# Optimization experiments

Measured on AMD Instinct MI355X. Metric: run time of the kernel, lower is better.

Reference implementation:

```python
import jax, jax.numpy as jnp
import numpy as np
from jax import lax

EPS = 1e-5

def _conv(x, w, stride=1, pad=0, groups=1):
    return lax.conv_general_dilated(
        x, w, (stride, stride), ((pad, pad), (pad, pad)),
        dimension_numbers=('NCHW', 'OIHW', 'NCHW'),
        feature_group_count=groups)

def _bn(x, gamma, beta):
    # BatchNorm2d, training-mode batch statistics (biased variance)
    mean = jnp.mean(x, axis=(0, 2, 3), keepdims=True)
    var = jnp.var(x, axis=(0, 2, 3), keepdims=True)
    xn = (x - mean) * lax.rsqrt(var + EPS)
    return xn * gamma[None, :, None, None] + beta[None, :, None, None]

def _silu(x):
    return x * jax.nn.sigmoid(x)

def setup_inputs() -> dict:
    key = jax.random.key(0)
    ks = jax.random.split(key, 20)
    B, C, H, W = 16, 128, 128, 128
    L2 = 100
    s = 0.05
    d = {
        'x': jax.random.normal(ks[0], (B, C, H, W), jnp.float32),
        'dce_output': jax.random.normal(ks[1], (B, L2, C), jnp.float32),
        # per-channel 3x3 convs fused as one depthwise conv [C,1,3,3]
        'dw_conv': jax.random.normal(ks[2], (C, 1, 3, 3), jnp.float32) * s,
        'W_dce1': jax.random.normal(ks[3], (L2 * C, C), jnp.float32) * s,
        'b_dce1': jnp.zeros((C,), jnp.float32),
        'W_dce2': jax.random.normal(ks[4], (C, C), jnp.float32) * s,
        'b_dce2': jnp.zeros((C,), jnp.float32),
        'W_sh': jax.random.normal(ks[5], (C, C // 2), jnp.float32) * s,
        'b_sh': jnp.zeros((C // 2,), jnp.float32),
        'W_ex': jax.random.normal(ks[6], (C // 2, C), jnp.float32) * s,
        'b_ex': jnp.zeros((C,), jnp.float32),
        'conv1_w': jax.random.normal(ks[7], (C, C, 3, 3), jnp.float32) * s,
        'bn1_g': jnp.ones((C,), jnp.float32),
        'bn1_b': jnp.zeros((C,), jnp.float32),
        'conv2_w': jax.random.normal(ks[8], (C, C, 1, 1), jnp.float32) * s,
        'bn2_g': jnp.ones((C,), jnp.float32),
        'bn2_b': jnp.zeros((C,), jnp.float32),
        'sc_w': jax.random.normal(ks[9], (C, C, 1, 1), jnp.float32) * s,
        'bnsc_g': jnp.ones((C,), jnp.float32),
        'bnsc_b': jnp.zeros((C,), jnp.float32),
    }
    return d

def reference(x, dce_output, dw_conv, W_dce1, b_dce1, W_dce2, b_dce2,
              W_sh, b_sh, W_ex, b_ex, conv1_w, bn1_g, bn1_b,
              conv2_w, bn2_g, bn2_b, sc_w, bnsc_g, bnsc_b):
    B, C, H, W = x.shape
    stride = 1
    # DCE FFN: Linear -> GELU(exact) -> Linear
    dce_flat = dce_output.reshape(B, -1)
    h = jax.nn.gelu(dce_flat @ W_dce1 + b_dce1, approximate=False)
    dce_features = h @ W_dce2 + b_dce2  # [B, C]
    # per-channel 3x3 conv + global avg pool, fused as depthwise conv
    sp = _conv(x, dw_conv, stride=1, pad=1, groups=C)
    spatial_features = jnp.mean(sp, axis=(2, 3))  # [B, C]
    # SE-style modulation
    m = dce_features * spatial_features
    shrunk = jax.nn.gelu(m @ W_sh + b_sh, approximate=False)
    mod_w = jax.nn.sigmoid(shrunk @ W_ex + b_ex)  # [B, C]
    xm = x * mod_w[:, :, None, None]
    # ResBlock
    bb = _bn(_conv(xm, conv1_w, stride=stride, pad=1), bn1_g, bn1_b)
    bb = _silu(bb)
    bb = _bn(_conv(bb, conv2_w, stride=1, pad=0), bn2_g, bn2_b)
    sc = _bn(_conv(xm, sc_w, stride=stride, pad=0), bnsc_g, bnsc_b)
    return _silu(bb + sc)
```

## Files before the change

kernel.cpp:

```cpp
#include <hip/hip_runtime.h>
#include <hip/hip_bf16.h>

typedef _Float16 f16;
typedef __attribute__((ext_vector_type(8))) _Float16 f16x8;
typedef __attribute__((ext_vector_type(4))) _Float16 f16x4;
typedef __attribute__((ext_vector_type(4))) float f32x4;

__device__ __forceinline__ float geluf(float x) {
    return 0.5f * x * (1.0f + erff(x * 0.70710678118654752440f));
}
__device__ __forceinline__ float sigmf(float x) { return 1.0f / (1.0f + __expf(-x)); }

#define NB 16
#define NC 128
#define NH 128
#define NW 128
#define PLANE (NH * NW)
#define NSTAT 262144.0f

__device__ __align__(16) f16 g_Wc[9 * 4 * 128 * 32];
__device__ __align__(16) f16 g_Wsc[4 * 128 * 32];
__device__ __align__(16) f16 g_W2[4 * 128 * 32];
__device__ __align__(16) f16 g_xmT[(size_t)16 * 128 * 4 * 130 * 32];
__device__ __align__(16) f16 g_y1T[(size_t)16 * 128 * 4 * 128 * 32];
__device__ __align__(16) f16 g_bbT[(size_t)16 * 128 * 4 * 128 * 32];

__global__ __launch_bounds__(256) void k_wprep(const float* __restrict__ c1w,
                                               const float* __restrict__ scw,
                                               const float* __restrict__ c2w) {
    int i = blockIdx.x * 256 + threadIdx.x;
    if (i < 147456) {
        int tap = i / 16384;
        int rem = i - tap * 16384;
        int chunk = rem >> 12;
        int r2 = rem & 4095;
        int co = r2 >> 5;
        int cil = r2 & 31;
        int ci = chunk * 32 + cil;
        g_Wc[i] = (f16)c1w[((size_t)co * 128 + ci) * 9 + tap];
    } else if (i < 163840) {
        int j = i - 147456;
        int chunk = j >> 12;
        int r2 = j & 4095;
        int co = r2 >> 5;
        int cil = r2 & 31;
        g_Wsc[j] = (f16)scw[(size_t)co * 128 + chunk * 32 + cil];
    } else if (i < 180224) {
        int j = i - 163840;
        int chunk = j >> 12;
        int r2 = j & 4095;
        int co = r2 >> 5;
        int cil = j & 31;
        g_W2[j] = (f16)c2w[(size_t)co * 128 + chunk * 32 + cil];
    }
}

__global__ __launch_bounds__(256) void k_dce1(const float* __restrict__ dce,
                                              const float* __restrict__ W1,
                                              float* __restrict__ dh) {
    int ks = blockIdx.x;
    int kbase = ks * 200;
    int t = threadIdx.x;
    __shared__ float sdce[16][256];
    for (int e = t; e < 4096; e += 256) {
        int bb = e >> 8, k = e & 255;
        if (k < 200) sdce[bb][k] = dce[(size_t)bb * 12800 + kbase + k];
    }
    __syncthreads();
    int j = t & 127;
    int bg = t >> 7;
    float accs[8];
#pragma unroll
    for (int i = 0; i < 8; ++i) accs[i] = 0.0f;
    for (int k = 0; k < 200; ++k) {
        float wv = W1[((size_t)(kbase + k)) * 128 + j];
#pragma unroll
        for (int bb = 0; bb < 8; ++bb) accs[bb] += sdce[bg * 8 + bb][k] * wv;
    }
#pragma unroll
    for (int bb = 0; bb < 8; ++bb)
        atomicAdd(&dh[(bg * 8 + bb) * 128 + j], accs[bb]);
}

__global__ __launch_bounds__(128) void k_dce2(const float* __restrict__ dh,
                                              const float* __restrict__ b1,
                                              const float* __restrict__ W2,
                                              const float* __restrict__ b2,
                                              float* __restrict__ feat) {
    int b = blockIdx.x, j = threadIdx.x;
    __shared__ float sh[128];
    sh[j] = geluf(dh[b * 128 + j] + b1[j]);
    __syncthreads();
    float acc = b2[j];
    for (int k = 0; k < 128; ++k) acc += sh[k] * W2[k * 128 + j];
    feat[b * 128 + j] = acc;
}

__global__ __launch_bounds__(256) void k_spatial(const float* __restrict__ x,
                                                 const float* __restrict__ dw,
                                                 float* __restrict__ spat) {
    int bc = blockIdx.x;
    int t = threadIdx.x;
    const float* p = x + (size_t)bc * PLANE;
    float f = 0, r0 = 0, r1 = 0, c0 = 0, c1 = 0;
    for (int i = t; i < PLANE; i += 256) {
        float v = p[i];
        int row = i >> 7, col = i & 127;
        f += v;
        if (row == 0) r0 += v;
        if (row == 127) r1 += v;
        if (col == 0) c0 += v;
        if (col == 127) c1 += v;
    }
#pragma unroll
    for (int o = 1; o < 64; o <<= 1) {
        f  += __shfl_xor(f, o);
        r0 += __shfl_xor(r0, o);
        r1 += __shfl_xor(r1, o);
        c0 += __shfl_xor(c0, o);
        c1 += __shfl_xor(c1, o);
    }
    __shared__ float wr[4][5];
    int wid = t >> 6;
    if ((t & 63) == 0) {
        wr[wid][0] = f; wr[wid][1] = r0; wr[wid][2] = r1; wr[wid][3] = c0; wr[wid][4] = c1;
    }
    __syncthreads();
    if (t == 0) {
        float full = 0, row0 = 0, row127 = 0, col0 = 0, col127 = 0;
#pragma unroll
        for (int w = 0; w < 4; ++w) {
            full += wr[w][0]; row0 += wr[w][1]; row127 += wr[w][2];
            col0 += wr[w][3]; col127 += wr[w][4];
        }
        int c = bc & 127;
        float x00 = p[0];
        float x0e = p[127];
        float xe0 = p[127 * 128];
        float xee = p[127 * 128 + 127];
        float acc = 0.0f;
        for (int kh = 0; kh < 3; ++kh)
            for (int kw = 0; kw < 3; ++kw) {
                int dh_ = kh - 1, dwv = kw - 1;
                float T = full;
                if (dh_ == -1) T -= row127;
                else if (dh_ == 1) T -= row0;
                if (dwv == -1) T -= col127;
                else if (dwv == 1) T -= col0;
                if (dh_ == -1 && dwv == -1) T += xee;
                if (dh_ == -1 && dwv == 1) T += xe0;
                if (dh_ == 1 && dwv == -1) T += x0e;
                if (dh_ == 1 && dwv == 1) T += x00;
                acc += dw[c * 9 + kh * 3 + kw] * T;
            }
        spat[bc] = acc * (1.0f / 16384.0f);
    }
}

__global__ __launch_bounds__(128) void k_mod(const float* __restrict__ feat,
                                             const float* __restrict__ spat,
                                             const float* __restrict__ Wsh,
                                             const float* __restrict__ bsh,
                                             const float* __restrict__ Wex,
                                             const float* __restrict__ bex,
                                             float* __restrict__ mod) {
    int b = blockIdx.x, t = threadIdx.x;
    __shared__ float sm[128], ssh[64];
    sm[t] = feat[b * 128 + t] * spat[b * 128 + t];
    __syncthreads();
    if (t < 64) {
        float acc = bsh[t];
        for (int c = 0; c < 128; ++c) acc += sm[c] * Wsh[c * 64 + t];
        ssh[t] = geluf(acc);
    }
    __syncthreads();
    float acc = bex[t];
    for (int k = 0; k < 64; ++k) acc += ssh[k] * Wex[k * 128 + t];
    mod[b * 128 + t] = sigmf(acc);
}

__global__ __launch_bounds__(256) void k_xprep(const float* __restrict__ x,
                                               const float* __restrict__ mod) {
    int bid = blockIdx.x;
    int h = bid & 127;
    int b = bid >> 7;
    int t = threadIdx.x;
    __shared__ float sx[32][133];

    for (int chunk = 0; chunk < 4; ++chunk) {
        __syncthreads();
#pragma unroll
        for (int it = 0; it < 4; ++it) {
            int ci = it * 8 + (t >> 5);
            int w4 = t & 31;
            int cig = chunk * 32 + ci;
            float4 v = *(const float4*)&x[(((size_t)b * 128 + cig) * 128 + h) * 128 + w4 * 4];
            float m = mod[b * 128 + cig];
            sx[ci][w4 * 4 + 0] = v.x * m;
            sx[ci][w4 * 4 + 1] = v.y * m;
            sx[ci][w4 * 4 + 2] = v.z * m;
            sx[ci][w4 * 4 + 3] = v.w * m;
        }
        __syncthreads();
        f16* dstc = g_xmT + (((size_t)(b * 128 + h)) * 4 + chunk) * 4160;
        for (int g = t; g < 520; g += 256) {
            int s = g >> 2, c8 = g & 3;
            f16x8 o;
            if (s == 0 || s == 129) {
#pragma unroll
                for (int j = 0; j < 8; ++j) o[j] = (f16)0.f;
            } else {
#pragma unroll
                for (int j = 0; j < 8; ++j) o[j] = (f16)sx[c8 * 8 + j][s - 1];
            }
            *(f16x8*)(dstc + s * 32 + c8 * 8) = o;
        }
    }
}

__global__ __launch_bounds__(256, 2) void k_conv1m(float* __restrict__ stats) {
    int orig = blockIdx.x;
    int sw = (orig & 7) * 256 + (orig >> 3);
    int h = sw & 127;
    int b = sw >> 7;
    int t = threadIdx.x;
    int lane = t & 63;
    int wv = t >> 6;
    int l15 = lane & 15, lg = lane >> 4;
    int co_half = (wv >> 1) * 64;
    int w_half = (wv & 1) * 64;

    __shared__ f16 xs[3][130][40];

    f32x4 acc[4][4];
#pragma unroll
    for (int ct = 0; ct < 4; ++ct)
#pragma unroll
        for (int wt = 0; wt < 4; ++wt) acc[ct][wt] = (f32x4){0.f, 0.f, 0.f, 0.f};

    f16x8 z8;
#pragma unroll
    for (int j = 0; j < 8; ++j) z8[j] = (f16)0.f;

    f16x8 st[7];

#pragma unroll
    for (int i = 0; i < 7; ++i) {
        int g = t + i * 256;
        if (g < 1560) {
            int r = g / 520;
            int q = g - r * 520;
            int s = q >> 2, c8 = q & 3;
            int hr = h + r - 1;
            st[i] = z8;
            if ((unsigned)hr < 128u)
                st[i] = *(const f16x8*)(g_xmT + (((size_t)(b * 128 + hr)) * 4 + 0) * 4160 + s * 32 + c8 * 8);
        }
    }
#pragma unroll
    for (int i = 0; i < 7; ++i) {
        int g = t + i * 256;
        if (g < 1560) {
            int r = g / 520;
            int q = g - r * 520;
            *(f16x8*)&xs[r][q >> 2][(q & 3) * 8] = st[i];
        }
    }
    __syncthreads();

    for (int chunk = 0; chunk < 4; ++chunk) {
        if (chunk < 3) {
#pragma unroll
            for (int i = 0; i < 7; ++i) {
                int g = t + i * 256;
                if (g < 1560) {
                    int r = g / 520;
                    int q = g - r * 520;
                    int s = q >> 2, c8 = q & 3;
                    int hr = h + r - 1;
                    st[i] = z8;
                    if ((unsigned)hr < 128u)
                        st[i] = *(const f16x8*)(g_xmT + (((size_t)(b * 128 + hr)) * 4 + chunk + 1) * 4160 + s * 32 + c8 * 8);
                }
            }
        }

#pragma unroll
        for (int tap = 0; tap < 9; ++tap) {
            const int kh = tap / 3, kw = tap - kh * 3;
            f16x8 af[4], bf[4];
#pragma unroll
            for (int ct = 0; ct < 4; ++ct)
                af[ct] = *(const f16x8*)(g_Wc + ((size_t)(tap * 4 + chunk) * 128 + co_half + ct * 16 + l15) * 32 + lg * 8);
#pragma unroll
            for (int wt = 0; wt < 4; ++wt)
                bf[wt] = *(const f16x8*)&xs[kh][w_half + wt * 16 + l15 + kw][lg * 8];
#pragma unroll
            for (int ct = 0; ct < 4; ++ct)
#pragma unroll
                for (int wt = 0; wt < 4; ++wt)
                    acc[ct][wt] = __builtin_amdgcn_mfma_f32_16x16x32_f16(
                        af[ct], bf[wt], acc[ct][wt], 0, 0, 0);
        }

        __syncthreads();
        if (chunk < 3) {
#pragma unroll
            for (int i = 0; i < 7; ++i) {
                int g = t + i * 256;
                if (g < 1560) {
                    int r = g / 520;
                    int q = g - r * 520;
                    *(f16x8*)&xs[r][q >> 2][(q & 3) * 8] = st[i];
                }
            }
            __syncthreads();
        }
    }

#pragma unroll
    for (int ct = 0; ct < 4; ++ct) {
        int cog = (wv >> 1) * 2 + (ct >> 1);
        int col = (ct & 1) * 16 + lg * 4;
#pragma unroll
        for (int wt = 0; wt < 4; ++wt) {
            int w = w_half + wt * 16 + l15;
            f16x4 pk;
            pk[0] = (f16)acc[ct][wt][0];
            pk[1] = (f16)acc[ct][wt][1];
            pk[2] = (f16)acc[ct][wt][2];
            pk[3] = (f16)acc[ct][wt][3];
            *(f16x4*)(g_y1T + ((((size_t)(b * 128 + h)) * 4 + cog) * 128 + w) * 32 + col) = pk;
        }
#pragma unroll
        for (int r = 0; r < 4; ++r) {
            int co = co_half + ct * 16 + lg * 4 + r;
            float s = 0, q = 0;
#pragma unroll
            for (int wt = 0; wt < 4; ++wt) {
                float v = acc[ct][wt][r];
                s += v; q += v * v;
            }
#pragma unroll
            for (int o = 1; o < 16; o <<= 1) {
                s += __shfl_xor(s, o);
                q += __shfl_xor(q, o);
            }
            if (l15 == 0) {
                atomicAdd(&stats[co], s);
                atomicAdd(&stats[128 + co], q);
            }
        }
    }
}

__global__ __launch_bounds__(128) void k_fin1(const float* __restrict__ stats,
                                              const float* __restrict__ g1, const float* __restrict__ be1,
                                              float* __restrict__ coef) {
    int t = threadIdx.x;
    const float inv = 1.0f / NSTAT;
    float m = stats[t] * inv;
    float v = stats[128 + t] * inv - m * m;
    float a = g1[t] * rsqrtf(v + 1e-5f);
    coef[t] = a;
    coef[128 + t] = be1[t] - m * a;
}

__global__ __launch_bounds__(256, 2) void k_conv2m(const float* __restrict__ coef,
                                                   float* __restrict__ stats) {
    int bid = blockIdx.x;
    int h = bid & 127;
    int b = bid >> 7;
    int t = threadIdx.x;
    int lane = t & 63;
    int wv = t >> 6;
    int l15 = lane & 15, lg = lane >> 4;
    int co_half = (wv >> 1) * 64;
    int w_half = (wv & 1) * 64;

    f32x4 acc[4][4], asc[4][4];
#pragma unroll
    for (int ct = 0; ct < 4; ++ct)
#pragma unroll
        for (int wt = 0; wt < 4; ++wt) {
            acc[ct][wt] = (f32x4){0.f, 0.f, 0.f, 0.f};
            asc[ct][wt] = (f32x4){0.f, 0.f, 0.f, 0.f};
        }

    for (int chunk = 0; chunk < 4; ++chunk) {
        float ca[8], cc[8];
#pragma unroll
        for (int j = 0; j < 8; ++j) {
            int ci = chunk * 32 + lg * 8 + j;
            ca[j] = coef[ci];
            cc[j] = coef[128 + ci];
        }
        f16x8 bfr[4], bx[4];
#pragma unroll
        for (int wt = 0; wt < 4; ++wt) {
            int w = w_half + wt * 16 + l15;
            f16x8 raw = *(const f16x8*)(g_y1T + ((((size_t)(b * 128 + h)) * 4 + chunk) * 128 + w) * 32 + lg * 8);
#pragma unroll
            for (int j = 0; j < 8; ++j) {
                float v = ca[j] * (float)raw[j] + cc[j];
                bfr[wt][j] = (f16)(v * sigmf(v));
            }
            bx[wt] = *(const f16x8*)(g_xmT + (((size_t)(b * 128 + h)) * 4 + chunk) * 4160 + (w + 1) * 32 + lg * 8);
        }
        if (wv < 2) {
#pragma unroll
            for (int wt = 0; wt < 4; ++wt) {
                int w = w_half + wt * 16 + l15;
                *(f16x8*)(g_bbT + ((((size_t)(b * 128 + h)) * 4 + chunk) * 128 + w) * 32 + lg * 8) = bfr[wt];
            }
        }
        f16x8 af[4], sf[4];
#pragma unroll
        for (int ct = 0; ct < 4; ++ct) {
            af[ct] = *(const f16x8*)(g_W2 + ((size_t)chunk * 128 + co_half + ct * 16 + l15) * 32 + lg * 8);
            sf[ct] = *(const f16x8*)(g_Wsc + ((size_t)chunk * 128 + co_half + ct * 16 + l15) * 32 + lg * 8);
        }
#pragma unroll
        for (int ct = 0; ct < 4; ++ct)
#pragma unroll
            for (int wt = 0; wt < 4; ++wt) {
                acc[ct][wt] = __builtin_amdgcn_mfma_f32_16x16x32_f16(
                    af[ct], bfr[wt], acc[ct][wt], 0, 0, 0);
                asc[ct][wt] = __builtin_amdgcn_mfma_f32_16x16x32_f16(
                    sf[ct], bx[wt], asc[ct][wt], 0, 0, 0);
            }
    }

#pragma unroll
    for (int ct = 0; ct < 4; ++ct) {
#pragma unroll
        for (int r = 0; r < 4; ++r) {
            int co = co_half + ct * 16 + lg * 4 + r;
            float s = 0, q = 0, ss = 0, qq = 0;
#pragma unroll
            for (int wt = 0; wt < 4; ++wt) {
                float v = acc[ct][wt][r];
                s += v; q += v * v;
                float u = asc[ct][wt][r];
                ss += u; qq += u * u;
            }
#pragma unroll
            for (int o = 1; o < 16; o <<= 1) {
                s += __shfl_xor(s, o);
                q += __shfl_xor(q, o);
                ss += __shfl_xor(ss, o);
                qq += __shfl_xor(qq, o);
            }
            if (l15 == 0) {
                atomicAdd(&stats[512 + co], s);
                atomicAdd(&stats[640 + co], q);
                atomicAdd(&stats[256 + co], ss);
                atomicAdd(&stats[384 + co], qq);
            }
        }
    }
}

__global__ __launch_bounds__(256) void k_fin2(const float* __restrict__ stats,
                                              const float* __restrict__ g2, const float* __restrict__ be2,
                                              const float* __restrict__ gsc, const float* __restrict__ bsc,
                                              float* __restrict__ coef) {
    int t = threadIdx.x;
    const float inv = 1.0f / NSTAT;
    if (t < 128) {
        float m = stats[512 + t] * inv;
        float v = stats[640 + t] * inv - m * m;
        float a = g2[t] * rsqrtf(v + 1e-5f);
        coef[512 + t] = a;
        coef[640 + t] = be2[t] - m * a;
    } else {
        int c = t - 128;
        float m = stats[256 + c] * inv;
        float v = stats[384 + c] * inv - m * m;
        float a = gsc[c] * rsqrtf(v + 1e-5f);
        coef[256 + c] = a;
        coef[384 + c] = bsc[c] - m * a;
    }
}

__global__ __launch_bounds__(256, 2) void k_final(float* __restrict__ out,
                                                  const float* __restrict__ coef) {
    int bid = blockIdx.x;
    int h = bid & 127;
    int b = bid >> 7;
    int t = threadIdx.x;
    int lane = t & 63;
    int wv = t >> 6;
    int l15 = lane & 15, lg = lane >> 4;
    int co_half = (wv >> 1) * 64;
    int w_half = (wv & 1) * 64;

    f32x4 acc[4][4], asc[4][4];
#pragma unroll
    for (int ct = 0; ct < 4; ++ct)
#pragma unroll
        for (int wt = 0; wt < 4; ++wt) {
            acc[ct][wt] = (f32x4){0.f, 0.f, 0.f, 0.f};
            asc[ct][wt] = (f32x4){0.f, 0.f, 0.f, 0.f};
        }

    for (int chunk = 0; chunk < 4; ++chunk) {
        f16x8 bf[4], bx[4], af[4], sf[4];
#pragma unroll
        for (int wt = 0; wt < 4; ++wt) {
            int w = w_half + wt * 16 + l15;
            bf[wt] = *(const f16x8*)(g_bbT + ((((size_t)(b * 128 + h)) * 4 + chunk) * 128 + w) * 32 + lg * 8);
            bx[wt] = *(const f16x8*)(g_xmT + (((size_t)(b * 128 + h)) * 4 + chunk) * 4160 + (w + 1) * 32 + lg * 8);
        }
#pragma unroll
        for (int ct = 0; ct < 4; ++ct) {
            af[ct] = *(const f16x8*)(g_W2 + ((size_t)chunk * 128 + co_half + ct * 16 + l15) * 32 + lg * 8);
            sf[ct] = *(const f16x8*)(g_Wsc + ((size_t)chunk * 128 + co_half + ct * 16 + l15) * 32 + lg * 8);
        }
#pragma unroll
        for (int ct = 0; ct < 4; ++ct)
#pragma unroll
            for (int wt = 0; wt < 4; ++wt) {
                acc[ct][wt] = __builtin_amdgcn_mfma_f32_16x16x32_f16(
                    af[ct], bf[wt], acc[ct][wt], 0, 0, 0);
                asc[ct][wt] = __builtin_amdgcn_mfma_f32_16x16x32_f16(
                    sf[ct], bx[wt], asc[ct][wt], 0, 0, 0);
            }
    }

#pragma unroll
    for (int ct = 0; ct < 4; ++ct) {
#pragma unroll
        for (int r = 0; r < 4; ++r) {
            int co = co_half + ct * 16 + lg * 4 + r;
            float a2 = coef[512 + co], c2 = coef[640 + co];
            float as = coef[256 + co], cs = coef[384 + co];
#pragma unroll
            for (int wt = 0; wt < 4; ++wt) {
                float v = a2 * acc[ct][wt][r] + c2 + as * asc[ct][wt][r] + cs;
                v = v * sigmf(v);
                out[(((size_t)b * 128 + co) * 128 + h) * 128 + w_half + wt * 16 + l15] = v;
            }
        }
    }
}

extern "C" void kernel_launch(void* const* d_in, const int* in_sizes, int n_in,
                              void* d_out, int out_size, void* d_ws, size_t ws_size,
                              hipStream_t stream) {
    (void)in_sizes; (void)n_in; (void)out_size; (void)ws_size;
    const float* x    = (const float*)d_in[0];
    const float* dce  = (const float*)d_in[1];
    const float* dwc  = (const float*)d_in[2];
    const float* W1   = (const float*)d_in[3];
    const float* b1   = (const float*)d_in[4];
    const float* W2d  = (const float*)d_in[5];
    const float* b2d  = (const float*)d_in[6];
    const float* Wsh  = (const float*)d_in[7];
    const float* bsh  = (const float*)d_in[8];
    const float* Wex  = (const float*)d_in[9];
    const float* bex  = (const float*)d_in[10];
    const float* c1w  = (const float*)d_in[11];
    const float* g1   = (const float*)d_in[12];
    const float* be1  = (const float*)d_in[13];
    const float* c2w  = (const float*)d_in[14];
    const float* g2   = (const float*)d_in[15];
    const float* be2  = (const float*)d_in[16];
    const float* scw  = (const float*)d_in[17];
    const float* gsc  = (const float*)d_in[18];
    const float* bsc  = (const float*)d_in[19];

    float* F = (float*)d_ws;
    float* dh    = F;
    float* stats = F + 2048;
    float* coef  = F + 2816;
    float* feat  = F + 3584;
    float* spat  = F + 5632;
    float* md    = F + 7680;

    float* out = (float*)d_out;

    hipMemsetAsync(F, 0, (2048 + 768) * sizeof(float), stream);

    k_wprep<<<704, 256, 0, stream>>>(c1w, scw, c2w);
    k_dce1<<<64, 256, 0, stream>>>(dce, W1, dh);
    k_dce2<<<16, 128, 0, stream>>>(dh, b1, W2d, b2d, feat);
    k_spatial<<<2048, 256, 0, stream>>>(x, dwc, spat);
    k_mod<<<16, 128, 0, stream>>>(feat, spat, Wsh, bsh, Wex, bex, md);
    k_xprep<<<2048, 256, 0, stream>>>(x, md);
    k_conv1m<<<2048, 256, 0, stream>>>(stats);
    k_fin1<<<1, 128, 0, stream>>>(stats, g1, be1, coef);
    k_conv2m<<<2048, 256, 0, stream>>>(coef, stats);
    k_fin2<<<1, 256, 0, stream>>>(stats, g2, be2, gsc, bsc, coef);
    k_final<<<2048, 256, 0, stream>>>(out, coef);
}
```

Baseline: 1.346 ms.

## Read conv1 input directly from global, raise occupancy, swizzle blocks, split DCE1

The conv1 kernel no longer stages the three input rows in shared memory. Each wave loads its MFMA B fragments straight from global (L2/L1) and substitutes zeros for out-of-range rows. Dropping the staging and its barriers allows a launch bound of 3 blocks per SM. The block-index swizzle already used in conv1 is applied to conv2 and the final kernel, and the DCE first linear layer is split into 128 smaller K slices for more parallelism. In exchange, conv1 reissues global loads per tap with no shared-memory reuse across waves, and more atomics land on the DCE accumulator.

Measured after the change: 1.266 ms. -5.9%, faster.

```diff
diff --git a/kernel.cpp b/kernel.cpp
--- a/kernel.cpp
+++ b/kernel.cpp
@@ -59,12 +59,12 @@
                                               const float* __restrict__ W1,
                                               float* __restrict__ dh) {
     int ks = blockIdx.x;
-    int kbase = ks * 200;
-    int t = threadIdx.x;
-    __shared__ float sdce[16][256];
-    for (int e = t; e < 4096; e += 256) {
-        int bb = e >> 8, k = e & 255;
-        if (k < 200) sdce[bb][k] = dce[(size_t)bb * 12800 + kbase + k];
+    int kbase = ks * 100;
+    int t = threadIdx.x;
+    __shared__ float sdce[16][100];
+    for (int e = t; e < 1600; e += 256) {
+        int bb = e / 100, k = e - bb * 100;
+        sdce[bb][k] = dce[(size_t)bb * 12800 + kbase + k];
     }
     __syncthreads();
     int j = t & 127;
@@ -72,7 +72,7 @@
     float accs[8];
 #pragma unroll
     for (int i = 0; i < 8; ++i) accs[i] = 0.0f;
-    for (int k = 0; k < 200; ++k) {
+    for (int k = 0; k < 100; ++k) {
         float wv = W1[((size_t)(kbase + k)) * 128 + j];
 #pragma unroll
         for (int bb = 0; bb < 8; ++bb) accs[bb] += sdce[bg * 8 + bb][k] * wv;
@@ -218,7 +218,7 @@
     }
 }
 
-__global__ __launch_bounds__(256, 2) void k_conv1m(float* __restrict__ stats) {
+__global__ __launch_bounds__(256, 3) void k_conv1m(float* __restrict__ stats) {
     int orig = blockIdx.x;
     int sw = (orig & 7) * 256 + (orig >> 3);
     int h = sw & 127;
@@ -230,8 +230,6 @@
     int co_half = (wv >> 1) * 64;
     int w_half = (wv & 1) * 64;
 
-    __shared__ f16 xs[3][130][40];
-
     f32x4 acc[4][4];
 #pragma unroll
     for (int ct = 0; ct < 4; ++ct)
@@ -242,49 +240,17 @@
 #pragma unroll
     for (int j = 0; j < 8; ++j) z8[j] = (f16)0.f;
 
-    f16x8 st[7];
-
-#pragma unroll
-    for (int i = 0; i < 7; ++i) {
-        int g = t + i * 256;
-        if (g < 1560) {
-            int r = g / 520;
-            int q = g - r * 520;
-            int s = q >> 2, c8 = q & 3;
-            int hr = h + r - 1;
-            st[i] = z8;
-            if ((unsigned)hr < 128u)
-                st[i] = *(const f16x8*)(g_xmT + (((size_t)(b * 128 + hr)) * 4 + 0) * 4160 + s * 32 + c8 * 8);
-        }
-    }
-#pragma unroll
-    for (int i = 0; i < 7; ++i) {
-        int g = t + i * 256;
-        if (g < 1560) {
-            int r = g / 520;
-            int q = g - r * 520;
-            *(f16x8*)&xs[r][q >> 2][(q & 3) * 8] = st[i];
-        }
-    }
-    __syncthreads();
-
+    const f16* xrow[3];
+    bool rok[3];
+#pragma unroll
+    for (int r = 0; r < 3; ++r) {
+        int hr = h + r - 1;
+        rok[r] = ((unsigned)hr < 128u);
+        xrow[r] = g_xmT + ((size_t)(b * 128 + (rok[r] ? hr : 0))) * 4 * 4160;
+    }
+
+#pragma unroll
     for (int chunk = 0; chunk < 4; ++chunk) {
-        if (chunk < 3) {
-#pragma unroll
-            for (int i = 0; i < 7; ++i) {
-                int g = t + i * 256;
-                if (g < 1560) {
-                    int r = g / 520;
-                    int q = g - r * 520;
-                    int s = q >> 2, c8 = q & 3;
-                    int hr = h + r - 1;
-                    st[i] = z8;
-                    if ((unsigned)hr < 128u)
-                        st[i] = *(const f16x8*)(g_xmT + (((size_t)(b * 128 + hr)) * 4 + chunk + 1) * 4160 + s * 32 + c8 * 8);
-                }
-            }
-        }
-
 #pragma unroll
         for (int tap = 0; tap < 9; ++tap) {
             const int kh = tap / 3, kw = tap - kh * 3;
@@ -292,29 +258,21 @@
 #pragma unroll
             for (int ct = 0; ct < 4; ++ct)
                 af[ct] = *(const f16x8*)(g_Wc + ((size_t)(tap * 4 + chunk) * 128 + co_half + ct * 16 + l15) * 32 + lg * 8);
-#pragma unroll
-            for (int wt = 0; wt < 4; ++wt)
-                bf[wt] = *(const f16x8*)&xs[kh][w_half + wt * 16 + l15 + kw][lg * 8];
+            if (rok[kh]) {
+#pragma unroll
+                for (int wt = 0; wt < 4; ++wt)
+                    bf[wt] = *(const f16x8*)(xrow[kh] + (size_t)chunk * 4160
+                                             + (w_half + wt * 16 + l15 + kw) * 32 + lg * 8);
+            } else {
+#pragma unroll
+                for (int wt = 0; wt < 4; ++wt) bf[wt] = z8;
+            }
 #pragma unroll
             for (int ct = 0; ct < 4; ++ct)
 #pragma unroll
                 for (int wt = 0; wt < 4; ++wt)
                     acc[ct][wt] = __builtin_amdgcn_mfma_f32_16x16x32_f16(
                         af[ct], bf[wt], acc[ct][wt], 0, 0, 0);
-        }
-
-        __syncthreads();
-        if (chunk < 3) {
-#pragma unroll
-            for (int i = 0; i < 7; ++i) {
-                int g = t + i * 256;
-                if (g < 1560) {
-                    int r = g / 520;
-                    int q = g - r * 520;
-                    *(f16x8*)&xs[r][q >> 2][(q & 3) * 8] = st[i];
-                }
-            }
-            __syncthreads();
         }
     }
 
@@ -368,9 +326,10 @@
 
 __global__ __launch_bounds__(256, 2) void k_conv2m(const float* __restrict__ coef,
                                                    float* __restrict__ stats) {
-    int bid = blockIdx.x;
-    int h = bid & 127;
-    int b = bid >> 7;
+    int orig = blockIdx.x;
+    int sw = (orig & 7) * 256 + (orig >> 3);
+    int h = sw & 127;
+    int b = sw >> 7;
     int t = threadIdx.x;
     int lane = t & 63;
     int wv = t >> 6;
@@ -485,9 +444,10 @@
 
 __global__ __launch_bounds__(256, 2) void k_final(float* __restrict__ out,
                                                   const float* __restrict__ coef) {
-    int bid = blockIdx.x;
-    int h = bid & 127;
-    int b = bid >> 7;
+    int orig = blockIdx.x;
+    int sw = (orig & 7) * 256 + (orig >> 3);
+    int h = sw & 127;
+    int b = sw >> 7;
     int t = threadIdx.x;
     int lane = t & 63;
     int wv = t >> 6;
@@ -583,7 +543,7 @@
     hipMemsetAsync(F, 0, (2048 + 768) * sizeof(float), stream);
 
     k_wprep<<<704, 256, 0, stream>>>(c1w, scw, c2w);
-    k_dce1<<<64, 256, 0, stream>>>(dce, W1, dh);
+    k_dce1<<<128, 256, 0, stream>>>(dce, W1, dh);
     k_dce2<<<16, 128, 0, stream>>>(dh, b1, W2d, b2d, feat);
     k_spatial<<<2048, 256, 0, stream>>>(x, dwc, spat);
     k_mod<<<16, 128, 0, stream>>>(feat, spat, Wsh, bsh, Wex, bex, md);
```
